# Optimization experiments

Hardware: AMD Instinct MI355X
Metric: run time of the kernel (lower is better)

## Reference

```python
import jax, jax.numpy as jnp
import numpy as np

BLOCK_SIZE = 256
N_EMBED = 384
HEAD_SIZE = 64


def setup_inputs() -> dict:
    key = jax.random.key(0)
    kx, kq, kk, kv = jax.random.split(key, 4)
    B, T = 256, 256
    x = jax.random.normal(kx, (B, T, N_EMBED), dtype=jnp.float32)
    # nn.Linear(n_embed, head_size, bias=False): y = x @ W.T with W [head, embed].
    # We store the transposed weight [embed, head] so forward is x @ W.
    scale = 1.0 / np.sqrt(N_EMBED)
    Wq = jax.random.normal(kq, (N_EMBED, HEAD_SIZE), dtype=jnp.float32) * scale
    Wk = jax.random.normal(kk, (N_EMBED, HEAD_SIZE), dtype=jnp.float32) * scale
    Wv = jax.random.normal(kv, (N_EMBED, HEAD_SIZE), dtype=jnp.float32) * scale
    return {"x": x, "Wq": Wq, "Wk": Wk, "Wv": Wv}


def reference(x, Wq, Wk, Wv):
    B, T, C = x.shape  # C == N_EMBED
    q = jnp.einsum('btc,ch->bth', x, Wq)
    k = jnp.einsum('btc,ch->bth', x, Wk)
    v = jnp.einsum('btc,ch->bth', x, Wv)
    # NOTE: original scales by 1/sqrt(C) where C = embed dim (384), not head_size.
    wei = jnp.einsum('bth,bsh->bts', q, k) / jnp.sqrt(jnp.float32(C))
    causal = jnp.tril(jnp.ones((T, T), dtype=bool))
    wei = jnp.where(causal, wei, -jnp.inf)
    wei = jax.nn.softmax(wei, axis=-1)
    # dropout is identity in eval mode (reference is deterministic)
    out = jnp.einsum('bts,bsh->bth', wei, v)
    return out
```

## Files before the change

kernel.cpp:

```cpp
#include <hip/hip_runtime.h>


typedef short s16x8 __attribute__((ext_vector_type(8)));
typedef float f32x4 __attribute__((ext_vector_type(4)));
typedef float f32x2 __attribute__((ext_vector_type(2)));
typedef unsigned u32x4 __attribute__((ext_vector_type(4)));
typedef __bf16 bf16x2t __attribute__((ext_vector_type(2)));

#define MFMA16(a, b, c) __builtin_amdgcn_mfma_f32_16x16x32_bf16((a), (b), (c), 0, 0, 0)

__device__ __forceinline__ unsigned short f2bf(float f) {
  return __builtin_bit_cast(unsigned short, (__bf16)f);
}
__device__ __forceinline__ unsigned cvt2(float a, float b) {
  f32x2 t; t[0] = a; t[1] = b;
  bf16x2t r = __builtin_convertvector(t, bf16x2t);
  return __builtin_bit_cast(unsigned, r);
}
__device__ __forceinline__ s16x8 cvt8(float4 a, float4 b) {
  u32x4 u;
  u[0] = cvt2(a.x, a.y); u[1] = cvt2(a.z, a.w);
  u[2] = cvt2(b.x, b.y); u[3] = cvt2(b.z, b.w);
  return __builtin_bit_cast(s16x8, u);
}
__device__ __forceinline__ s16x8 asm_frag(uint2 t0, uint2 t1, int laneA, bool hi) {
  unsigned r0a = __shfl(t0.x, laneA),      r0b = __shfl(t0.y, laneA);
  unsigned r0c = __shfl(t0.x, laneA + 16), r0d = __shfl(t0.y, laneA + 16);
  unsigned r1a = __shfl(t1.x, laneA),      r1b = __shfl(t1.y, laneA);
  unsigned r1c = __shfl(t1.x, laneA + 16), r1d = __shfl(t1.y, laneA + 16);
  u32x4 u;
  u[0] = hi ? r1a : r0a; u[1] = hi ? r1b : r0b;
  u[2] = hi ? r1c : r0c; u[3] = hi ? r1d : r0d;
  return __builtin_bit_cast(s16x8, u);
}

__global__ __launch_bounds__(256) void wcvt(
    const float* __restrict__ Wq, const float* __restrict__ Wk,
    const float* __restrict__ Wv, unsigned short* __restrict__ Wt_sw) {
  int idx = blockIdx.x * 256 + threadIdx.x;
  int j = idx & 7;
  int c = idx >> 3;
  int n15 = c & 15;
  int q4 = (c >> 4) & 3;
  int g = c >> 6;
  int nt = g % 12;
  int kc = g / 12;
  int n = nt * 16 + n15;
  int kk = kc * 32 + q4 * 8 + j;
  const float* src = (n < 64) ? Wq : (n < 128) ? Wk : Wv;
  float v = src[kk * 64 + (n & 63)];
  if (n < 64) v *= 0.05103103630798287f;
  Wt_sw[idx] = f2bf(v);
}

__global__ __launch_bounds__(1024, 4) void fused_attn(
    const float* __restrict__ x, const unsigned short* __restrict__ Wt_sw,
    float* __restrict__ out) {
  __shared__ __align__(16) unsigned short k_l[16384];
  __shared__ __align__(16) unsigned short v_l[16384];
  __shared__ __align__(16) unsigned short w_l[12288];
  const int b = blockIdx.x;
  const int tid = threadIdx.x;
  const int wv = tid >> 6;
  const int lane = tid & 63;
  const int n15 = lane & 15;
  const int q4 = lane >> 4;

  f32x4 acc[12];
#pragma unroll
  for (int i = 0; i < 12; ++i) acc[i] = (f32x4){0.f, 0.f, 0.f, 0.f};

  const float* xp = x + ((long)b * 256 + wv * 16 + n15) * 384 + q4 * 8;
  float4 f0a = *reinterpret_cast<const float4*>(xp);
  float4 f0b = *reinterpret_cast<const float4*>(xp + 4);
  float4 f1a = *reinterpret_cast<const float4*>(xp + 32);
  float4 f1b = *reinterpret_cast<const float4*>(xp + 36);

  const uint4* Wv4 = reinterpret_cast<const uint4*>(Wt_sw);
  uint4* wl4 = reinterpret_cast<uint4*>(w_l);
  uint4 wreg;
  if (tid < 768) wreg = Wv4[tid];

  for (int kc = 0; kc < 12; ++kc) {
    if (tid < 768) wl4[(kc & 1) * 768 + tid] = wreg;
    __syncthreads();
    if (kc < 11 && tid < 768) wreg = Wv4[(kc + 1) * 768 + tid];
    const int nkc = (kc < 10) ? kc + 2 : 11;
    float4 pa = *reinterpret_cast<const float4*>(xp + nkc * 32);
    float4 pb = *reinterpret_cast<const float4*>(xp + nkc * 32 + 4);

    s16x8 xa = cvt8(f0a, f0b);
    const unsigned short* wbuf = w_l + (kc & 1) * 6144;
#pragma unroll
    for (int nt = 0; nt < 12; ++nt) {
      s16x8 wf = *reinterpret_cast<const s16x8*>(&wbuf[nt * 512 + lane * 8]);
      if (nt < 8) acc[nt] = MFMA16(wf, xa, acc[nt]);
      else        acc[nt] = MFMA16(xa, wf, acc[nt]);
    }
    f0a = f1a; f0b = f1b; f1a = pa; f1b = pb;
  }

  uint2 pkq[4];
#pragma unroll
  for (int mt = 0; mt < 4; ++mt) {
    pkq[mt].x = cvt2(acc[mt][0], acc[mt][1]);
    pkq[mt].y = cvt2(acc[mt][2], acc[mt][3]);
  }
#pragma unroll
  for (int mt = 0; mt < 4; ++mt) {
    const int off = ((wv * 2 + (mt >> 1)) * 64 + (2 * (mt & 1) + (q4 >> 1)) * 16 + n15) * 8
                    + (q4 & 1) * 4;
    uint2 sk;
    sk.x = cvt2(acc[4 + mt][0], acc[4 + mt][1]);
    sk.y = cvt2(acc[4 + mt][2], acc[4 + mt][3]);
    *reinterpret_cast<uint2*>(&k_l[off]) = sk;
  }
  const int s0 = wv * 16 + q4 * 4;
#pragma unroll
  for (int nt = 0; nt < 4; ++nt) {
    const int off = (((s0 >> 5) * 4 + nt) * 64 + ((s0 >> 3) & 3) * 16 + n15) * 8 + (s0 & 7);
    uint2 sv;
    sv.x = cvt2(acc[8 + nt][0], acc[8 + nt][1]);
    sv.y = cvt2(acc[8 + nt][2], acc[8 + nt][3]);
    *reinterpret_cast<uint2*>(&v_l[off]) = sv;
  }

  const int laneA = ((q4 & 1) << 5) + n15;
  const bool hi = (q4 >> 1) != 0;
  const s16x8 qf0 = asm_frag(pkq[0], pkq[1], laneA, hi);
  const s16x8 qf1 = asm_frag(pkq[2], pkq[3], laneA, hi);
  __syncthreads();

  const int qt = wv;
  const f32x4 zf = (f32x4){0.f, 0.f, 0.f, 0.f};
  f32x4 O[4];
#pragma unroll
  for (int nt = 0; nt < 4; ++nt) O[nt] = zf;
  float psum = 0.f;
  const int nk = (qt + 2) >> 1;
#pragma unroll 8
  for (int kc = 0; kc < 8; ++kc) {
    if (kc >= nk) break;
    const int ct0 = 2 * kc;
    const bool has1 = (ct0 + 1 <= qt);
    s16x8 kf0 = *reinterpret_cast<const s16x8*>(&k_l[(ct0 * 2 + 0) * 512 + lane * 8]);
    s16x8 kf1 = *reinterpret_cast<const s16x8*>(&k_l[(ct0 * 2 + 1) * 512 + lane * 8]);
    f32x4 a0 = MFMA16(kf0, qf0, zf);
    f32x4 a1 = MFMA16(kf1, qf1, zf);
    uint2 t0, t1;
    {
      f32x4 s = a0 + a1;
      const bool diag = (ct0 == qt);
      float p[4];
#pragma unroll
      for (int e = 0; e < 4; ++e) {
        p[e] = (diag && (q4 * 4 + e > n15)) ? 0.f : __expf(s[e]);
        psum += p[e];
      }
      t0.x = cvt2(p[0], p[1]); t0.y = cvt2(p[2], p[3]);
    }
    if (has1) {
      const int ct1 = ct0 + 1;
      s16x8 kg0 = *reinterpret_cast<const s16x8*>(&k_l[(ct1 * 2 + 0) * 512 + lane * 8]);
      s16x8 kg1 = *reinterpret_cast<const s16x8*>(&k_l[(ct1 * 2 + 1) * 512 + lane * 8]);
      f32x4 b0 = MFMA16(kg0, qf0, zf);
      f32x4 b1 = MFMA16(kg1, qf1, zf);
      f32x4 s = b0 + b1;
      const bool diag = (ct1 == qt);
      float p[4];
#pragma unroll
      for (int e = 0; e < 4; ++e) {
        p[e] = (diag && (q4 * 4 + e > n15)) ? 0.f : __expf(s[e]);
        psum += p[e];
      }
      t1.x = cvt2(p[0], p[1]); t1.y = cvt2(p[2], p[3]);
    } else {
      t1 = make_uint2(0u, 0u);
    }
    s16x8 pf = asm_frag(t0, t1, laneA, hi);
#pragma unroll
    for (int nt = 0; nt < 4; ++nt) {
      s16x8 vf = *reinterpret_cast<const s16x8*>(&v_l[(kc * 4 + nt) * 512 + lane * 8]);
      O[nt] = MFMA16(pf, vf, O[nt]);
    }
  }
  psum += __shfl_xor(psum, 16);
  psum += __shfl_xor(psum, 32);
  const float rn_col = 1.0f / psum;
  float rnm[4];
#pragma unroll
  for (int e = 0; e < 4; ++e) rnm[e] = __shfl(rn_col, q4 * 4 + e);
#pragma unroll
  for (int nt = 0; nt < 4; ++nt)
#pragma unroll
    for (int e = 0; e < 4; ++e)
      out[(size_t)(b * 256 + qt * 16 + q4 * 4 + e) * 64 + nt * 16 + n15] = O[nt][e] * rnm[e];
}

extern "C" void kernel_launch(void* const* d_in, const int* in_sizes, int n_in,
                              void* d_out, int out_size, void* d_ws, size_t ws_size,
                              hipStream_t stream) {
  const float* x  = (const float*)d_in[0];
  const float* Wq = (const float*)d_in[1];
  const float* Wk = (const float*)d_in[2];
  const float* Wv = (const float*)d_in[3];
  float* out = (float*)d_out;

  unsigned short* Wt_sw = (unsigned short*)d_ws;

  wcvt<<<288, 256, 0, stream>>>(Wq, Wk, Wv, Wt_sw);
  fused_attn<<<256, 1024, 0, stream>>>(x, Wt_sw, out);
}
```

Measured before the change: 166.0 us.

## Preload all projection weights into LDS once and balance causal tiles across SIMDs

Replaces the per-k-chunk double-buffered weight staging, which needed a barrier every iteration, with a single up-front load of all 144 KB of bf16 weights into a unified LDS buffer followed by one barrier. K/V tiles then alias the same memory, so their stores are deferred until after a barrier. It also remaps wave-to-query-tile assignment so causal workloads are balanced across SIMDs. The cost is much larger LDS use per block and an extra barrier before the K/V writes.

```diff
diff --git a/kernel.cpp b/kernel.cpp
--- a/kernel.cpp
+++ b/kernel.cpp
@@ -56,41 +56,40 @@
 __global__ __launch_bounds__(1024, 4) void fused_attn(
     const float* __restrict__ x, const unsigned short* __restrict__ Wt_sw,
     float* __restrict__ out) {
-  __shared__ __align__(16) unsigned short k_l[16384];
-  __shared__ __align__(16) unsigned short v_l[16384];
-  __shared__ __align__(16) unsigned short w_l[12288];
+  __shared__ __align__(16) unsigned short smem[73728];
+  unsigned short* const k_l = smem;
+  unsigned short* const v_l = smem + 16384;
   const int b = blockIdx.x;
   const int tid = threadIdx.x;
   const int wv = tid >> 6;
   const int lane = tid & 63;
   const int n15 = lane & 15;
   const int q4 = lane >> 4;
+  const int tt = ((wv >> 3) & 1) * 8 + (((wv >> 2) & 1) ? 7 - (wv & 3) : (wv & 3));
 
   f32x4 acc[12];
 #pragma unroll
   for (int i = 0; i < 12; ++i) acc[i] = (f32x4){0.f, 0.f, 0.f, 0.f};
 
-  const float* xp = x + ((long)b * 256 + wv * 16 + n15) * 384 + q4 * 8;
+  const float* xp = x + ((long)b * 256 + tt * 16 + n15) * 384 + q4 * 8;
   float4 f0a = *reinterpret_cast<const float4*>(xp);
   float4 f0b = *reinterpret_cast<const float4*>(xp + 4);
   float4 f1a = *reinterpret_cast<const float4*>(xp + 32);
   float4 f1b = *reinterpret_cast<const float4*>(xp + 36);
 
   const uint4* Wv4 = reinterpret_cast<const uint4*>(Wt_sw);
-  uint4* wl4 = reinterpret_cast<uint4*>(w_l);
-  uint4 wreg;
-  if (tid < 768) wreg = Wv4[tid];
+  uint4* wl4 = reinterpret_cast<uint4*>(smem);
+#pragma unroll
+  for (int i = 0; i < 9; ++i) wl4[i * 1024 + tid] = Wv4[i * 1024 + tid];
+  __syncthreads();
 
   for (int kc = 0; kc < 12; ++kc) {
-    if (tid < 768) wl4[(kc & 1) * 768 + tid] = wreg;
-    __syncthreads();
-    if (kc < 11 && tid < 768) wreg = Wv4[(kc + 1) * 768 + tid];
     const int nkc = (kc < 10) ? kc + 2 : 11;
     float4 pa = *reinterpret_cast<const float4*>(xp + nkc * 32);
     float4 pb = *reinterpret_cast<const float4*>(xp + nkc * 32 + 4);
 
     s16x8 xa = cvt8(f0a, f0b);
-    const unsigned short* wbuf = w_l + (kc & 1) * 6144;
+    const unsigned short* wbuf = smem + kc * 6144;
 #pragma unroll
     for (int nt = 0; nt < 12; ++nt) {
       s16x8 wf = *reinterpret_cast<const s16x8*>(&wbuf[nt * 512 + lane * 8]);
@@ -106,32 +105,37 @@
     pkq[mt].x = cvt2(acc[mt][0], acc[mt][1]);
     pkq[mt].y = cvt2(acc[mt][2], acc[mt][3]);
   }
+  uint2 sk[4], sv[4];
+  int koff[4], voff[4];
 #pragma unroll
   for (int mt = 0; mt < 4; ++mt) {
-    const int off = ((wv * 2 + (mt >> 1)) * 64 + (2 * (mt & 1) + (q4 >> 1)) * 16 + n15) * 8
-                    + (q4 & 1) * 4;
-    uint2 sk;
-    sk.x = cvt2(acc[4 + mt][0], acc[4 + mt][1]);
-    sk.y = cvt2(acc[4 + mt][2], acc[4 + mt][3]);
-    *reinterpret_cast<uint2*>(&k_l[off]) = sk;
-  }
-  const int s0 = wv * 16 + q4 * 4;
+    koff[mt] = ((tt * 2 + (mt >> 1)) * 64 + (2 * (mt & 1) + (q4 >> 1)) * 16 + n15) * 8
+               + (q4 & 1) * 4;
+    sk[mt].x = cvt2(acc[4 + mt][0], acc[4 + mt][1]);
+    sk[mt].y = cvt2(acc[4 + mt][2], acc[4 + mt][3]);
+  }
+  const int s0 = tt * 16 + q4 * 4;
 #pragma unroll
   for (int nt = 0; nt < 4; ++nt) {
-    const int off = (((s0 >> 5) * 4 + nt) * 64 + ((s0 >> 3) & 3) * 16 + n15) * 8 + (s0 & 7);
-    uint2 sv;
-    sv.x = cvt2(acc[8 + nt][0], acc[8 + nt][1]);
-    sv.y = cvt2(acc[8 + nt][2], acc[8 + nt][3]);
-    *reinterpret_cast<uint2*>(&v_l[off]) = sv;
-  }
-
+    voff[nt] = (((s0 >> 5) * 4 + nt) * 64 + ((s0 >> 3) & 3) * 16 + n15) * 8 + (s0 & 7);
+    sv[nt].x = cvt2(acc[8 + nt][0], acc[8 + nt][1]);
+    sv[nt].y = cvt2(acc[8 + nt][2], acc[8 + nt][3]);
+  }
   const int laneA = ((q4 & 1) << 5) + n15;
   const bool hi = (q4 >> 1) != 0;
   const s16x8 qf0 = asm_frag(pkq[0], pkq[1], laneA, hi);
   const s16x8 qf1 = asm_frag(pkq[2], pkq[3], laneA, hi);
+
   __syncthreads();
-
-  const int qt = wv;
+#pragma unroll
+  for (int mt = 0; mt < 4; ++mt)
+    *reinterpret_cast<uint2*>(&k_l[koff[mt]]) = sk[mt];
+#pragma unroll
+  for (int nt = 0; nt < 4; ++nt)
+    *reinterpret_cast<uint2*>(&v_l[voff[nt]]) = sv[nt];
+  __syncthreads();
+
+  const int qt = tt;
   const f32x4 zf = (f32x4){0.f, 0.f, 0.f, 0.f};
   f32x4 O[4];
 #pragma unroll
```

New measurement: 166.4 us. Within noise of the previous version (+0.3%).
